# Kernel tuning notes

Hardware: AMD Instinct MI355X
Metric: run time of the kernel (lower is better)

Reference implementation:

```python
import jax, jax.numpy as jnp
import numpy as np

D_MODEL = 768
NUM_HEADS = 12
D_K = D_MODEL // NUM_HEADS


def setup_inputs() -> dict:
    key = jax.random.key(0)
    k1, k2, k3 = jax.random.split(key, 3)
    s = 1.0 / np.sqrt(D_MODEL)
    return {
        "x": jax.random.normal(k1, (4, 2048, D_MODEL), dtype=jnp.float32),
        "W_qkv": jax.random.normal(k2, (D_MODEL, 3 * D_MODEL), dtype=jnp.float32) * s,
        "b_qkv": jnp.zeros((3 * D_MODEL,), dtype=jnp.float32),
        "W_out": jax.random.normal(k3, (D_MODEL, D_MODEL), dtype=jnp.float32) * s,
        "b_out": jnp.zeros((D_MODEL,), dtype=jnp.float32),
    }


def reference(x, W_qkv, b_qkv, W_out, b_out):
    B, S, _ = x.shape
    # fused QKV projection: [B,S,3*d_model]
    qkv = x @ W_qkv + b_qkv
    # reshape to [B,S,H,3*d_k] then to [B,H,S,3*d_k] (matches torch permute)
    qkv = qkv.reshape(B, S, NUM_HEADS, 3 * D_K).transpose(0, 2, 1, 3)
    q, k, v = jnp.split(qkv, 3, axis=-1)  # each [B,H,S,d_k]
    scale = 1.0 / jnp.sqrt(jnp.float32(D_K))
    scores = jnp.einsum("bhqd,bhkd->bhqk", q, k) * scale
    attn = jax.nn.softmax(scores, axis=-1)
    context = jnp.einsum("bhqk,bhkd->bhqd", attn, v)
    context = context.transpose(0, 2, 1, 3).reshape(B, S, D_MODEL)
    return context @ W_out + b_out
```

## Files before the change

kernel.cpp:

```cpp
#include <hip/hip_runtime.h>
#include <hip/hip_bf16.h>
#include <math.h>

#define D_MODEL 768
#define NUM_HEADS 12
#define D_K 64
#define SEQ 2048
#define BATCH 4
#define QKV_N 2304

#define QSCALE 0.18033688011112042f

typedef _Float16 f16;
typedef f16 f16x4 __attribute__((ext_vector_type(4)));
typedef f16 f16x8 __attribute__((ext_vector_type(8)));
typedef float f32x4 __attribute__((ext_vector_type(4)));

#if __has_builtin(__builtin_amdgcn_exp2f)
#define EXP2F(x) __builtin_amdgcn_exp2f(x)
#else
#define EXP2F(x) __expf(0.6931471805599453f * (x))
#endif

__device__ __forceinline__ void gload_lds16(const f16* g, f16* l) {
  __builtin_amdgcn_global_load_lds(
      (const __attribute__((address_space(1))) void*)g,
      (__attribute__((address_space(3))) void*)l, 16, 0, 0);
}

__device__ inline void xcd_swizzle(int& bx, int& by) {
  const int nx = gridDim.x;
  const int nwg = nx * gridDim.y;
  const int bidlin = blockIdx.y * nx + blockIdx.x;
  const int cpx = nwg >> 3;
  const int wg = (bidlin & 7) * cpx + (bidlin >> 3);
  bx = wg % nx;
  by = wg / nx;
}

__global__ __launch_bounds__(256) void prep_x(const float* __restrict__ x,
                                              f16* __restrict__ xh) {
  const int idx = blockIdx.x * 256 + threadIdx.x;
#pragma unroll
  for (int i = 0; i < 2; ++i) {
    const size_t c = (size_t)idx + (size_t)i * 393216;
    const float4 a = *(const float4*)(x + c * 8);
    const float4 b = *(const float4*)(x + c * 8 + 4);
    f16x8 h = { (f16)a.x, (f16)a.y, (f16)a.z, (f16)a.w,
                (f16)b.x, (f16)b.y, (f16)b.z, (f16)b.w };
    *(f16x8*)(xh + c * 8) = h;
  }
}

__global__ __launch_bounds__(256) void prep_wt(const float* __restrict__ W,
                                               f16* __restrict__ Wt,
                                               int K, int N) {
  const int n0 = blockIdx.x * 64;
  const int k0 = blockIdx.y * 64;
  const int tid = threadIdx.x;
  __shared__ f16 t[64][72];

#pragma unroll
  for (int i = 0; i < 4; ++i) {
    const int slot = tid + i * 256;
    const int r = slot >> 4;
    const int c4 = (slot & 15) * 4;
    const float4 v = *(const float4*)(W + (size_t)(k0 + r) * N + n0 + c4);
    t[c4 + 0][r] = (f16)v.x;
    t[c4 + 1][r] = (f16)v.y;
    t[c4 + 2][r] = (f16)v.z;
    t[c4 + 3][r] = (f16)v.w;
  }
  __syncthreads();
#pragma unroll
  for (int i = 0; i < 2; ++i) {
    const int slot = tid + i * 256;
    const int n = slot >> 3;
    const int kc = (slot & 7) * 8;
    *(f16x8*)(Wt + (size_t)(n0 + n) * K + k0 + kc) = *(const f16x8*)(&t[n][kc]);
  }
}

#define GEMM_CORE(A_, B_, K_)                                               \
  __shared__ f16 Als[128 * 32];                                             \
  __shared__ f16 Bls[128 * 32];                                             \
  f32x4 acc[4][4];                                                          \
  _Pragma("unroll") for (int i = 0; i < 4; ++i)                             \
      _Pragma("unroll") for (int j = 0; j < 4; ++j)                         \
          acc[i][j] = (f32x4){0.f, 0.f, 0.f, 0.f};                          \
  const int sr = w * 32 + (lane >> 2);                                      \
  const int sc = (lane & 3) * 8;                                            \
  const f16* gA0 = A_ + (size_t)(bm + sr) * K_ + sc;                        \
  const f16* gA1 = gA0 + (size_t)16 * K_;                                   \
  const f16* gB0 = B_ + (size_t)(bn + sr) * K_ + sc;                        \
  const f16* gB1 = gB0 + (size_t)16 * K_;                                   \
  f16* lA0 = Als + (w * 32) * 32;                                           \
  f16* lA1 = lA0 + 16 * 32;                                                 \
  f16* lB0 = Bls + (w * 32) * 32;                                           \
  f16* lB1 = lB0 + 16 * 32;                                                 \
  for (int k0 = 0; k0 < K_; k0 += 32) {                                     \
    gload_lds16(gA0 + k0, lA0);                                             \
    gload_lds16(gA1 + k0, lA1);                                             \
    gload_lds16(gB0 + k0, lB0);                                             \
    gload_lds16(gB1 + k0, lB1);                                             \
    __syncthreads();                                                        \
    f16x8 af[4], bf[4];                                                     \
    _Pragma("unroll") for (int mi = 0; mi < 4; ++mi)                        \
        af[mi] = *(const f16x8*)(Als + (wr * 64 + mi * 16 + c) * 32 + g * 8); \
    _Pragma("unroll") for (int nj = 0; nj < 4; ++nj)                        \
        bf[nj] = *(const f16x8*)(Bls + (wc * 64 + nj * 16 + c) * 32 + g * 8); \
    _Pragma("unroll") for (int mi = 0; mi < 4; ++mi)                        \
        _Pragma("unroll") for (int nj = 0; nj < 4; ++nj)                    \
            acc[mi][nj] = __builtin_amdgcn_mfma_f32_16x16x32_f16(           \
                af[mi], bf[nj], acc[mi][nj], 0, 0, 0);                      \
    __syncthreads();                                                        \
  }

__global__ __launch_bounds__(256) void gemm_qkv(
    const f16* __restrict__ A, const f16* __restrict__ B,
    const float* __restrict__ bias,
    f16* __restrict__ Qh, f16* __restrict__ Kh, f16* __restrict__ Vt) {
  int bx, by;
  xcd_swizzle(bx, by);
  const int bm = by * 128;
  const int bn = bx * 128;
  const int tid = threadIdx.x;
  const int lane = tid & 63;
  const int w = tid >> 6;
  const int wr = w >> 1;
  const int wc = w & 1;
  const int c = lane & 15;
  const int g = lane >> 4;

  GEMM_CORE(A, B, 768)

  const int crow = g * 4;
  const int ccol = c;
#pragma unroll
  for (int nj = 0; nj < 4; ++nj) {
    const int col = bn + wc * 64 + nj * 16 + ccol;
    const int h = col / 192;
    const int rem = col - h * 192;
    const int sub = rem >> 6;
    const int d = rem & 63;
    const float bv = bias[col];
#pragma unroll
    for (int mi = 0; mi < 4; ++mi) {
      const int tok0 = bm + wr * 64 + mi * 16 + crow;
      const int b = tok0 >> 11;
      const int t0 = tok0 & 2047;
      const int bh = b * NUM_HEADS + h;
      if (sub == 2) {
        f16x4 pv = { (f16)(acc[mi][nj][0] + bv), (f16)(acc[mi][nj][1] + bv),
                     (f16)(acc[mi][nj][2] + bv), (f16)(acc[mi][nj][3] + bv) };
        *(f16x4*)(Vt + ((size_t)bh * 64 + d) * SEQ + t0) = pv;
      } else if (sub == 0) {
#pragma unroll
        for (int r = 0; r < 4; ++r)
          Qh[((size_t)bh * SEQ + t0 + r) * 64 + d] =
              (f16)((acc[mi][nj][r] + bv) * QSCALE);
      } else {
#pragma unroll
        for (int r = 0; r < 4; ++r)
          Kh[((size_t)bh * SEQ + t0 + r) * 64 + d] =
              (f16)(acc[mi][nj][r] + bv);
      }
    }
  }
}

__global__ __launch_bounds__(256) void gemm_out(
    const f16* __restrict__ A, const f16* __restrict__ B,
    const float* __restrict__ bias, float* __restrict__ C) {
  int bx, by;
  xcd_swizzle(bx, by);
  const int bm = by * 128;
  const int bn = bx * 128;
  const int tid = threadIdx.x;
  const int lane = tid & 63;
  const int w = tid >> 6;
  const int wr = w >> 1;
  const int wc = w & 1;
  const int c = lane & 15;
  const int g = lane >> 4;

  GEMM_CORE(A, B, 768)

  const int crow = g * 4;
  const int ccol = c;
#pragma unroll
  for (int nj = 0; nj < 4; ++nj) {
    const int col = bn + wc * 64 + nj * 16 + ccol;
    const float bv = bias[col];
#pragma unroll
    for (int mi = 0; mi < 4; ++mi) {
      const int rbase = bm + wr * 64 + mi * 16 + crow;
#pragma unroll
      for (int r = 0; r < 4; ++r) {
        C[(size_t)(rbase + r) * D_MODEL + col] = acc[mi][nj][r] + bv;
      }
    }
  }
}

__global__ __launch_bounds__(512, 6) void flash_attn_mfma(
    const f16* __restrict__ Qh, const f16* __restrict__ Kh,
    const f16* __restrict__ Vt, f16* __restrict__ ctxh) {
  const int qt = blockIdx.x, h = blockIdx.y, b = blockIdx.z;
  const int bh = b * NUM_HEADS + h;
  const int q0 = qt * 128;
  const int tid = threadIdx.x;
  const int lane = tid & 63;
  const int w = tid >> 6;
  const int c = lane & 15;
  const int g = lane >> 4;

  __shared__ f16 Ql[128 * 64];
  __shared__ f16 Kl[64 * 64];
  __shared__ f16 Vl[64 * 64];
  __shared__ f16 Pl[8][16 * 64];

  const f16* Kbase = Kh + (size_t)bh * SEQ * 64;
  const f16* Vbase = Vt + (size_t)bh * 64 * SEQ;

#pragma unroll
  for (int ii = 0; ii < 2; ++ii) {
    const int slot = tid + ii * 512;
    const int row = slot >> 3;
    const int g8 = (slot & 7) * 8;
    f16x8 hq = *(const f16x8*)(Qh + ((size_t)bh * SEQ + q0 + row) * 64 + g8);
    *(f16x8*)(Ql + row * 64 + (g8 ^ ((row & 7) << 3))) = hq;
  }
  {
    const int row = tid >> 3;
    const int g8 = (tid & 7) * 8;
    f16x8 hk = *(const f16x8*)(Kbase + (size_t)row * 64 + g8);
    *(f16x8*)(Kl + row * 64 + (g8 ^ ((row & 7) << 3))) = hk;
    f16x8 hv = *(const f16x8*)(Vbase + (size_t)row * SEQ + g8);
    *(f16x8*)(Vl + row * 64 + (g8 ^ ((row & 7) << 3))) = hv;
  }
  __syncthreads();

  f16x8 qf[2];
#pragma unroll
  for (int s = 0; s < 2; ++s) {
    const int row = w * 16 + c;
    qf[s] = *(const f16x8*)(Ql + row * 64 +
                            ((s * 32 + g * 8) ^ ((row & 7) << 3)));
  }

  f32x4 o[4];
  float m_ = -INFINITY, l_ = 0.f;
#pragma unroll
  for (int dt = 0; dt < 4; ++dt) o[dt] = (f32x4){0.f, 0.f, 0.f, 0.f};

  const int srow = tid >> 3;
  const int sg8 = (tid & 7) * 8;

  for (int kt = 0; kt < SEQ / 64; ++kt) {
    f16x8 nk, nv;
    const bool more = (kt + 1) < SEQ / 64;
    if (more) {
      nk = *(const f16x8*)(Kbase + (size_t)(kt + 1) * 64 * 64 +
                           (size_t)srow * 64 + sg8);
      nv = *(const f16x8*)(Vbase + (size_t)srow * SEQ + (kt + 1) * 64 + sg8);
    }

    f32x4 s_[4];
#pragma unroll
    for (int mt = 0; mt < 4; ++mt) s_[mt] = (f32x4){0.f, 0.f, 0.f, 0.f};

    __builtin_amdgcn_s_setprio(1);
#pragma unroll
    for (int s2 = 0; s2 < 2; ++s2) {
#pragma unroll
      for (int mt = 0; mt < 4; ++mt) {
        const int row = mt * 16 + c;
        const f16x8 kf = *(const f16x8*)(Kl + row * 64 +
                         ((s2 * 32 + g * 8) ^ ((row & 7) << 3)));
        s_[mt] = __builtin_amdgcn_mfma_f32_16x16x32_f16(
            kf, qf[s2], s_[mt], 0, 0, 0);
      }
    }
    __builtin_amdgcn_s_setprio(0);

    {
      float tm = -INFINITY;
#pragma unroll
      for (int mt = 0; mt < 4; ++mt)
#pragma unroll
        for (int r = 0; r < 4; ++r) tm = fmaxf(tm, s_[mt][r]);
      tm = fmaxf(tm, __shfl_xor(tm, 16));
      tm = fmaxf(tm, __shfl_xor(tm, 32));

      if (!__all(tm <= m_)) {
        const float mn = fmaxf(m_, tm);
        const float sc = EXP2F(m_ - mn);
        m_ = mn;
        l_ *= sc;
#pragma unroll
        for (int dt = 0; dt < 4; ++dt) o[dt] *= sc;
      }
      const float mn = m_;

      float rs = 0.f;
#pragma unroll
      for (int mt = 0; mt < 4; ++mt) {
        f32x4 e;
#pragma unroll
        for (int r = 0; r < 4; ++r) {
          e[r] = EXP2F(s_[mt][r] - mn);
          rs += e[r];
        }
        s_[mt] = e;
      }
      rs += __shfl_xor(rs, 16);
      rs += __shfl_xor(rs, 32);
      l_ += rs;

      const int prow = c;
#pragma unroll
      for (int mt = 0; mt < 4; ++mt) {
        f16x4 pk = { (f16)s_[mt][0], (f16)s_[mt][1],
                     (f16)s_[mt][2], (f16)s_[mt][3] };
        *(f16x4*)(&Pl[w][prow * 64 +
                         ((mt * 16 + g * 4) ^ ((prow & 7) << 3))]) = pk;
      }
    }

    __builtin_amdgcn_s_setprio(1);
#pragma unroll
    for (int s2 = 0; s2 < 2; ++s2) {
      const f16x8 pf = *(const f16x8*)(&Pl[w][c * 64 +
                        ((s2 * 32 + g * 8) ^ ((c & 7) << 3))]);
#pragma unroll
      for (int dt = 0; dt < 4; ++dt) {
        const int row = dt * 16 + c;
        const f16x8 vf = *(const f16x8*)(Vl + row * 64 +
                         ((s2 * 32 + g * 8) ^ ((row & 7) << 3)));
        o[dt] = __builtin_amdgcn_mfma_f32_16x16x32_f16(
            vf, pf, o[dt], 0, 0, 0);
      }
    }
    __builtin_amdgcn_s_setprio(0);

    __syncthreads();

    if (more) {
      *(f16x8*)(Kl + srow * 64 + (sg8 ^ ((srow & 7) << 3))) = nk;
      *(f16x8*)(Vl + srow * 64 + (sg8 ^ ((srow & 7) << 3))) = nv;
    }
    __syncthreads();
  }

  {
    const float inv = 1.f / l_;
    const int q = q0 + w * 16 + c;
#pragma unroll
    for (int dt = 0; dt < 4; ++dt) {
      f16x4 r4 = { (f16)(o[dt][0] * inv), (f16)(o[dt][1] * inv),
                   (f16)(o[dt][2] * inv), (f16)(o[dt][3] * inv) };
      *(f16x4*)(ctxh + ((size_t)(b * SEQ) + q) * D_MODEL + h * 64 +
                dt * 16 + g * 4) = r4;
    }
  }
}

extern "C" void kernel_launch(void* const* d_in, const int* in_sizes, int n_in,
                              void* d_out, int out_size, void* d_ws, size_t ws_size,
                              hipStream_t stream) {
  const float* x     = (const float*)d_in[0];
  const float* W_qkv = (const float*)d_in[1];
  const float* b_qkv = (const float*)d_in[2];
  const float* W_out = (const float*)d_in[3];
  const float* b_out = (const float*)d_in[4];
  float* out = (float*)d_out;

  const int M = BATCH * SEQ;
  const int BH = BATCH * NUM_HEADS;

  f16* xh   = (f16*)d_ws;
  f16* Wqt  = xh + (size_t)M * D_MODEL;
  f16* Wot  = Wqt + (size_t)QKV_N * D_MODEL;
  f16* Qh   = Wot + (size_t)D_MODEL * D_MODEL;
  f16* Kh   = Qh + (size_t)BH * SEQ * 64;
  f16* Vt   = Kh + (size_t)BH * SEQ * 64;
  f16* ctxh = Vt + (size_t)BH * SEQ * 64;

  dim3 block(256);

  hipLaunchKernelGGL(prep_x, dim3(1536), block, 0, stream, x, xh);
  hipLaunchKernelGGL(prep_wt, dim3(QKV_N / 64, D_MODEL / 64), block, 0, stream,
                     W_qkv, Wqt, D_MODEL, QKV_N);
  hipLaunchKernelGGL(prep_wt, dim3(D_MODEL / 64, D_MODEL / 64), block, 0, stream,
                     W_out, Wot, D_MODEL, D_MODEL);

  hipLaunchKernelGGL(gemm_qkv, dim3(QKV_N / 128, M / 128), block, 0, stream,
                     xh, Wqt, b_qkv, Qh, Kh, Vt);

  hipLaunchKernelGGL(flash_attn_mfma, dim3(SEQ / 128, NUM_HEADS, BATCH),
                     dim3(512), 0, stream, Qh, Kh, Vt, ctxh);

  hipLaunchKernelGGL(gemm_out, dim3(D_MODEL / 128, M / 128), block, 0, stream,
                     ctxh, Wot, b_out, out);
}
```

Before: 172.7 us.

## Merge prep kernels and process two K/V tiles per attention iteration

The three preprocessing launches (x conversion and two weight transposes) are merged into one kernel that dispatches on block index, which saves launch overhead. In flash attention, Q fragments are kept in registers after loading, so the Q shared-memory buffer is reused as a second K/V tile buffer. Each loop iteration now processes two 64-key tiles and prefetches the next two, halving the number of block-wide barriers per key. The cost is more live registers for the prefetched data, which could lower occupancy.

```diff
diff --git a/kernel.cpp b/kernel.cpp
--- a/kernel.cpp
+++ b/kernel.cpp
@@ -38,27 +38,40 @@
   by = wg / nx;
 }
 
-__global__ __launch_bounds__(256) void prep_x(const float* __restrict__ x,
-                                              f16* __restrict__ xh) {
-  const int idx = blockIdx.x * 256 + threadIdx.x;
-#pragma unroll
-  for (int i = 0; i < 2; ++i) {
-    const size_t c = (size_t)idx + (size_t)i * 393216;
-    const float4 a = *(const float4*)(x + c * 8);
-    const float4 b = *(const float4*)(x + c * 8 + 4);
-    f16x8 h = { (f16)a.x, (f16)a.y, (f16)a.z, (f16)a.w,
-                (f16)b.x, (f16)b.y, (f16)b.z, (f16)b.w };
-    *(f16x8*)(xh + c * 8) = h;
-  }
-}
-
-__global__ __launch_bounds__(256) void prep_wt(const float* __restrict__ W,
-                                               f16* __restrict__ Wt,
-                                               int K, int N) {
-  const int n0 = blockIdx.x * 64;
-  const int k0 = blockIdx.y * 64;
+__global__ __launch_bounds__(256) void prep_all(
+    const float* __restrict__ x, const float* __restrict__ Wq,
+    const float* __restrict__ Wo, f16* __restrict__ xh,
+    f16* __restrict__ Wqt, f16* __restrict__ Wot) {
+  const int bid = blockIdx.x;
   const int tid = threadIdx.x;
   __shared__ f16 t[64][72];
+
+  if (bid < 1536) {
+    const int idx = bid * 256 + tid;
+#pragma unroll
+    for (int i = 0; i < 2; ++i) {
+      const size_t c = (size_t)idx + (size_t)i * 393216;
+      const float4 a = *(const float4*)(x + c * 8);
+      const float4 b = *(const float4*)(x + c * 8 + 4);
+      f16x8 h = { (f16)a.x, (f16)a.y, (f16)a.z, (f16)a.w,
+                  (f16)b.x, (f16)b.y, (f16)b.z, (f16)b.w };
+      *(f16x8*)(xh + c * 8) = h;
+    }
+    return;
+  }
+
+  const float* W;
+  f16* Wt;
+  int K, N, n0, k0;
+  if (bid < 1968) {
+    const int tt = bid - 1536;
+    W = Wq; Wt = Wqt; K = 768; N = QKV_N;
+    n0 = (tt % 36) * 64; k0 = (tt / 36) * 64;
+  } else {
+    const int tt = bid - 1968;
+    W = Wo; Wt = Wot; K = 768; N = D_MODEL;
+    n0 = (tt % 12) * 64; k0 = (tt / 12) * 64;
+  }
 
 #pragma unroll
   for (int i = 0; i < 4; ++i) {
@@ -203,6 +216,68 @@
   }
 }
 
+#define COMPUTE_TILE(KL_, VL_)                                              \
+  {                                                                         \
+    f32x4 s_[4];                                                            \
+    _Pragma("unroll") for (int mt = 0; mt < 4; ++mt)                        \
+        s_[mt] = (f32x4){0.f, 0.f, 0.f, 0.f};                               \
+    __builtin_amdgcn_s_setprio(1);                                          \
+    _Pragma("unroll") for (int s2 = 0; s2 < 2; ++s2) {                      \
+      _Pragma("unroll") for (int mt = 0; mt < 4; ++mt) {                    \
+        const int row = mt * 16 + c;                                        \
+        const f16x8 kf = *(const f16x8*)(KL_ + row * 64 +                   \
+                         ((s2 * 32 + g * 8) ^ ((row & 7) << 3)));           \
+        s_[mt] = __builtin_amdgcn_mfma_f32_16x16x32_f16(                    \
+            kf, qf[s2], s_[mt], 0, 0, 0);                                   \
+      }                                                                     \
+    }                                                                       \
+    __builtin_amdgcn_s_setprio(0);                                          \
+    float tm = -INFINITY;                                                   \
+    _Pragma("unroll") for (int mt = 0; mt < 4; ++mt)                        \
+        _Pragma("unroll") for (int r = 0; r < 4; ++r)                       \
+            tm = fmaxf(tm, s_[mt][r]);                                      \
+    tm = fmaxf(tm, __shfl_xor(tm, 16));                                     \
+    tm = fmaxf(tm, __shfl_xor(tm, 32));                                     \
+    if (!__all(tm <= m_)) {                                                 \
+      const float mn2 = fmaxf(m_, tm);                                      \
+      const float sc2 = EXP2F(m_ - mn2);                                    \
+      m_ = mn2;                                                             \
+      l_ *= sc2;                                                            \
+      _Pragma("unroll") for (int dt = 0; dt < 4; ++dt) o[dt] *= sc2;        \
+    }                                                                       \
+    const float mn = m_;                                                    \
+    float rs = 0.f;                                                         \
+    _Pragma("unroll") for (int mt = 0; mt < 4; ++mt) {                      \
+      f32x4 e;                                                              \
+      _Pragma("unroll") for (int r = 0; r < 4; ++r) {                       \
+        e[r] = EXP2F(s_[mt][r] - mn);                                       \
+        rs += e[r];                                                         \
+      }                                                                     \
+      s_[mt] = e;                                                           \
+    }                                                                       \
+    rs += __shfl_xor(rs, 16);                                               \
+    rs += __shfl_xor(rs, 32);                                               \
+    l_ += rs;                                                               \
+    _Pragma("unroll") for (int mt = 0; mt < 4; ++mt) {                      \
+      f16x4 pk = { (f16)s_[mt][0], (f16)s_[mt][1],                          \
+                   (f16)s_[mt][2], (f16)s_[mt][3] };                        \
+      *(f16x4*)(&Pl[w][c * 64 + ((mt * 16 + g * 4) ^ ((c & 7) << 3))]) = pk;\
+    }                                                                       \
+    __builtin_amdgcn_s_setprio(1);                                          \
+    _Pragma("unroll") for (int s2 = 0; s2 < 2; ++s2) {                      \
+      const f16x8 pf = *(const f16x8*)(&Pl[w][c * 64 +                      \
+                        ((s2 * 32 + g * 8) ^ ((c & 7) << 3))]);             \
+      _Pragma("unroll") for (int dt = 0; dt < 4; ++dt) {                    \
+        const int row = dt * 16 + c;                                        \
+        const f16x8 vf = *(const f16x8*)(VL_ + row * 64 +                   \
+                         ((s2 * 32 + g * 8) ^ ((row & 7) << 3)));           \
+        o[dt] = __builtin_amdgcn_mfma_f32_16x16x32_f16(                     \
+            vf, pf, o[dt], 0, 0, 0);                                        \
+      }                                                                     \
+    }                                                                       \
+    __builtin_amdgcn_s_setprio(0);                                          \
+  }
+
 __global__ __launch_bounds__(512, 6) void flash_attn_mfma(
     const f16* __restrict__ Qh, const f16* __restrict__ Kh,
     const f16* __restrict__ Vt, f16* __restrict__ ctxh) {
@@ -215,13 +290,20 @@
   const int c = lane & 15;
   const int g = lane >> 4;
 
-  __shared__ f16 Ql[128 * 64];
+  __shared__ f16 QPl[128 * 64];
   __shared__ f16 Kl[64 * 64];
   __shared__ f16 Vl[64 * 64];
   __shared__ f16 Pl[8][16 * 64];
+  f16* Ql = QPl;
+  f16* KB = QPl;
+  f16* VB = QPl + 64 * 64;
 
   const f16* Kbase = Kh + (size_t)bh * SEQ * 64;
   const f16* Vbase = Vt + (size_t)bh * 64 * SEQ;
+
+  const int srow = tid >> 3;
+  const int sg8 = (tid & 7) * 8;
+  const int sswz = sg8 ^ ((srow & 7) << 3);
 
 #pragma unroll
   for (int ii = 0; ii < 2; ++ii) {
@@ -232,12 +314,10 @@
     *(f16x8*)(Ql + row * 64 + (g8 ^ ((row & 7) << 3))) = hq;
   }
   {
-    const int row = tid >> 3;
-    const int g8 = (tid & 7) * 8;
-    f16x8 hk = *(const f16x8*)(Kbase + (size_t)row * 64 + g8);
-    *(f16x8*)(Kl + row * 64 + (g8 ^ ((row & 7) << 3))) = hk;
-    f16x8 hv = *(const f16x8*)(Vbase + (size_t)row * SEQ + g8);
-    *(f16x8*)(Vl + row * 64 + (g8 ^ ((row & 7) << 3))) = hv;
+    f16x8 hk = *(const f16x8*)(Kbase + (size_t)srow * 64 + sg8);
+    *(f16x8*)(Kl + srow * 64 + sswz) = hk;
+    f16x8 hv = *(const f16x8*)(Vbase + (size_t)srow * SEQ + sg8);
+    *(f16x8*)(Vl + srow * 64 + sswz) = hv;
   }
   __syncthreads();
 
@@ -248,107 +328,42 @@
     qf[s] = *(const f16x8*)(Ql + row * 64 +
                             ((s * 32 + g * 8) ^ ((row & 7) << 3)));
   }
+  __syncthreads();
+
+  {
+    f16x8 hk = *(const f16x8*)(Kbase + (size_t)64 * 64 + (size_t)srow * 64 + sg8);
+    *(f16x8*)(KB + srow * 64 + sswz) = hk;
+    f16x8 hv = *(const f16x8*)(Vbase + (size_t)srow * SEQ + 64 + sg8);
+    *(f16x8*)(VB + srow * 64 + sswz) = hv;
+  }
+  __syncthreads();
 
   f32x4 o[4];
   float m_ = -INFINITY, l_ = 0.f;
 #pragma unroll
   for (int dt = 0; dt < 4; ++dt) o[dt] = (f32x4){0.f, 0.f, 0.f, 0.f};
 
-  const int srow = tid >> 3;
-  const int sg8 = (tid & 7) * 8;
-
-  for (int kt = 0; kt < SEQ / 64; ++kt) {
-    f16x8 nk, nv;
-    const bool more = (kt + 1) < SEQ / 64;
+  for (int pt = 0; pt < SEQ / 128; ++pt) {
+    f16x8 nkA, nvA, nkB, nvB;
+    const bool more = (pt + 1) < SEQ / 128;
     if (more) {
-      nk = *(const f16x8*)(Kbase + (size_t)(kt + 1) * 64 * 64 +
-                           (size_t)srow * 64 + sg8);
-      nv = *(const f16x8*)(Vbase + (size_t)srow * SEQ + (kt + 1) * 64 + sg8);
-    }
-
-    f32x4 s_[4];
-#pragma unroll
-    for (int mt = 0; mt < 4; ++mt) s_[mt] = (f32x4){0.f, 0.f, 0.f, 0.f};
-
-    __builtin_amdgcn_s_setprio(1);
-#pragma unroll
-    for (int s2 = 0; s2 < 2; ++s2) {
-#pragma unroll
-      for (int mt = 0; mt < 4; ++mt) {
-        const int row = mt * 16 + c;
-        const f16x8 kf = *(const f16x8*)(Kl + row * 64 +
-                         ((s2 * 32 + g * 8) ^ ((row & 7) << 3)));
-        s_[mt] = __builtin_amdgcn_mfma_f32_16x16x32_f16(
-            kf, qf[s2], s_[mt], 0, 0, 0);
-      }
-    }
-    __builtin_amdgcn_s_setprio(0);
-
-    {
-      float tm = -INFINITY;
-#pragma unroll
-      for (int mt = 0; mt < 4; ++mt)
-#pragma unroll
-        for (int r = 0; r < 4; ++r) tm = fmaxf(tm, s_[mt][r]);
-      tm = fmaxf(tm, __shfl_xor(tm, 16));
-      tm = fmaxf(tm, __shfl_xor(tm, 32));
-
-      if (!__all(tm <= m_)) {
-        const float mn = fmaxf(m_, tm);
-        const float sc = EXP2F(m_ - mn);
-        m_ = mn;
-        l_ *= sc;
-#pragma unroll
-        for (int dt = 0; dt < 4; ++dt) o[dt] *= sc;
-      }
-      const float mn = m_;
-
-      float rs = 0.f;
-#pragma unroll
-      for (int mt = 0; mt < 4; ++mt) {
-        f32x4 e;
-#pragma unroll
-        for (int r = 0; r < 4; ++r) {
-          e[r] = EXP2F(s_[mt][r] - mn);
-          rs += e[r];
-        }
-        s_[mt] = e;
-      }
-      rs += __shfl_xor(rs, 16);
-      rs += __shfl_xor(rs, 32);
-      l_ += rs;
-
-      const int prow = c;
-#pragma unroll
-      for (int mt = 0; mt < 4; ++mt) {
-        f16x4 pk = { (f16)s_[mt][0], (f16)s_[mt][1],
-                     (f16)s_[mt][2], (f16)s_[mt][3] };
-        *(f16x4*)(&Pl[w][prow * 64 +
-                         ((mt * 16 + g * 4) ^ ((prow & 7) << 3))]) = pk;
-      }
-    }
-
-    __builtin_amdgcn_s_setprio(1);
-#pragma unroll
-    for (int s2 = 0; s2 < 2; ++s2) {
-      const f16x8 pf = *(const f16x8*)(&Pl[w][c * 64 +
-                        ((s2 * 32 + g * 8) ^ ((c & 7) << 3))]);
-#pragma unroll
-      for (int dt = 0; dt < 4; ++dt) {
-        const int row = dt * 16 + c;
-        const f16x8 vf = *(const f16x8*)(Vl + row * 64 +
-                         ((s2 * 32 + g * 8) ^ ((row & 7) << 3)));
-        o[dt] = __builtin_amdgcn_mfma_f32_16x16x32_f16(
-            vf, pf, o[dt], 0, 0, 0);
-      }
-    }
-    __builtin_amdgcn_s_setprio(0);
+      const int tA = 2 * pt + 2, tB = 2 * pt + 3;
+      nkA = *(const f16x8*)(Kbase + (size_t)tA * 64 * 64 + (size_t)srow * 64 + sg8);
+      nvA = *(const f16x8*)(Vbase + (size_t)srow * SEQ + tA * 64 + sg8);
+      nkB = *(const f16x8*)(Kbase + (size_t)tB * 64 * 64 + (size_t)srow * 64 + sg8);
+      nvB = *(const f16x8*)(Vbase + (size_t)srow * SEQ + tB * 64 + sg8);
+    }
+
+    COMPUTE_TILE(Kl, Vl)
+    COMPUTE_TILE(KB, VB)
 
     __syncthreads();
 
     if (more) {
-      *(f16x8*)(Kl + srow * 64 + (sg8 ^ ((srow & 7) << 3))) = nk;
-      *(f16x8*)(Vl + srow * 64 + (sg8 ^ ((srow & 7) << 3))) = nv;
+      *(f16x8*)(Kl + srow * 64 + sswz) = nkA;
+      *(f16x8*)(Vl + srow * 64 + sswz) = nvA;
+      *(f16x8*)(KB + srow * 64 + sswz) = nkB;
+      *(f16x8*)(VB + srow * 64 + sswz) = nvB;
     }
     __syncthreads();
   }
@@ -389,11 +404,8 @@
 
   dim3 block(256);
 
-  hipLaunchKernelGGL(prep_x, dim3(1536), block, 0, stream, x, xh);
-  hipLaunchKernelGGL(prep_wt, dim3(QKV_N / 64, D_MODEL / 64), block, 0, stream,
-                     W_qkv, Wqt, D_MODEL, QKV_N);
-  hipLaunchKernelGGL(prep_wt, dim3(D_MODEL / 64, D_MODEL / 64), block, 0, stream,
-                     W_out, Wot, D_MODEL, D_MODEL);
+  hipLaunchKernelGGL(prep_all, dim3(2112), block, 0, stream,
+                     x, W_qkv, W_out, xh, Wqt, Wot);
 
   hipLaunchKernelGGL(gemm_qkv, dim3(QKV_N / 128, M / 128), block, 0, stream,
                      xh, Wqt, b_qkv, Qh, Kh, Vt);
```

New measurement: 178.1 us. 1.03x slower.
